# Kernel optimization log

Hardware: AMD Instinct MI355X
Metric: run time of the kernel (lower is better)

The kernel has to match this reference:

```python
import jax, jax.numpy as jnp
import numpy as np

B, N, F, H = 8, 2048, 64, 1

def setup_inputs() -> dict:
    key = jax.random.key(0)
    k1, k2, k3, k4 = jax.random.split(key, 4)
    return {
        "encode": jax.random.normal(k1, (B, N, F), dtype=jnp.float32),
        "kernel": jax.random.normal(k2, (F, H, F), dtype=jnp.float32) * 0.1,
        "attn_kernel_self": jax.random.normal(k3, (F, H, 1), dtype=jnp.float32) * 0.1,
        "attn_kernel_neighs": jax.random.normal(k4, (F, H, 1), dtype=jnp.float32) * 0.1,
    }

def reference(encode, kernel, attn_kernel_self, attn_kernel_neighs):
    # project: [B,N,F] x [F,H,F] -> [B,N,H,F]
    h = jnp.einsum('bni,iho->bnho', encode, kernel)
    # per-node scalar scores: [B,N,H,1]
    a_self = jnp.einsum('bnhi,iho->bnho', h, attn_kernel_self)
    a_neigh = jnp.einsum('bnhi,iho->bnho', h, attn_kernel_neighs)
    # transpose last three axes (...ABC -> ...CBA): [B,1,H,N]
    a_neigh_t = jnp.transpose(a_neigh, (0, 3, 2, 1))
    # broadcast-sum -> [B,N,H,N] dense logits, leaky_relu(alpha=0.2), softmax over neighbors
    logits = jax.nn.leaky_relu(a_self + a_neigh_t, negative_slope=0.2)
    coef = jax.nn.softmax(logits, axis=-1)
    # mean over heads (axis=2) -> [B,N,N]
    return jnp.mean(coef, axis=2)
```

## Files before the change

kernel.cpp:

```cpp
#include <hip/hip_runtime.h>

#define BB 8
#define NN 2048
#define FF 64

typedef float f32x4 __attribute__((ext_vector_type(4)));

__global__ __launch_bounds__(256) void scores_fused(const float* __restrict__ enc,
                                                    const float* __restrict__ kmat,
                                                    const float* __restrict__ aks,
                                                    const float* __restrict__ akn,
                                                    float* __restrict__ S,
                                                    float* __restrict__ T) {
    __shared__ float ws[FF], wn[FF];
    const int tid = threadIdx.x;
    if (tid < FF) {
        float s = 0.f, t = 0.f;
        #pragma unroll
        for (int o = 0; o < FF; ++o) {
            float k = kmat[tid * FF + o];
            s += k * aks[o];
            t += k * akn[o];
        }
        ws[tid] = s;
        wn[tid] = t;
    }
    __syncthreads();

    const int g = blockIdx.x * 256 + tid;
    const f32x4* e4 = (const f32x4*)(enc + (size_t)g * FF);
    const f32x4* w4 = (const f32x4*)ws;
    const f32x4* v4 = (const f32x4*)wn;
    float s = 0.f, t = 0.f;
    #pragma unroll
    for (int j = 0; j < FF / 4; ++j) {
        f32x4 e = e4[j];
        f32x4 w = w4[j];
        f32x4 v = v4[j];
        s += e.x * w.x + e.y * w.y + e.z * w.z + e.w * w.w;
        t += e.x * v.x + e.y * v.y + e.z * v.z + e.w * v.w;
    }
    S[g] = s;
    T[g] = t;
}

__device__ __forceinline__ float waveMax(float v) {
    #pragma unroll
    for (int o = 32; o > 0; o >>= 1) v = fmaxf(v, __shfl_xor(v, o, 64));
    return v;
}
__device__ __forceinline__ float waveSum(float v) {
    #pragma unroll
    for (int o = 32; o > 0; o >>= 1) v += __shfl_xor(v, o, 64);
    return v;
}

__global__ __launch_bounds__(256) void softmax_kernel(const float* __restrict__ S,
                                                      const float* __restrict__ T,
                                                      float* __restrict__ out) {
    const int wave = threadIdx.x >> 6;
    const int lane = threadIdx.x & 63;
    const int row  = blockIdx.x * 4 + wave;
    const int b    = row >> 11;

    const float s = S[row];
    const f32x4* t4 = (const f32x4*)(T + (size_t)b * NN);

    auto lk = [](float x) { return x > 0.f ? x : 0.2f * x; };

    f32x4 l[8];
    float m = -3.4e38f;
    #pragma unroll
    for (int j = 0; j < 8; ++j) {
        f32x4 t = t4[lane + 64 * j];
        l[j].x = lk(s + t.x); l[j].y = lk(s + t.y);
        l[j].z = lk(s + t.z); l[j].w = lk(s + t.w);
        m = fmaxf(m, fmaxf(fmaxf(l[j].x, l[j].y), fmaxf(l[j].z, l[j].w)));
    }
    m = waveMax(m);

    float ls = 0.f;
    #pragma unroll
    for (int j = 0; j < 8; ++j) {
        l[j].x = __expf(l[j].x - m); l[j].y = __expf(l[j].y - m);
        l[j].z = __expf(l[j].z - m); l[j].w = __expf(l[j].w - m);
        ls += (l[j].x + l[j].y) + (l[j].z + l[j].w);
    }
    ls = waveSum(ls);
    const float inv = 1.f / ls;

    f32x4* o4 = (f32x4*)(out + (size_t)row * NN);
    #pragma unroll
    for (int j = 0; j < 8; ++j) {
        f32x4 o;
        o.x = l[j].x * inv; o.y = l[j].y * inv;
        o.z = l[j].z * inv; o.w = l[j].w * inv;
        __builtin_nontemporal_store(o, &o4[lane + 64 * j]);
    }
}

extern "C" void kernel_launch(void* const* d_in, const int* in_sizes, int n_in,
                              void* d_out, int out_size, void* d_ws, size_t ws_size,
                              hipStream_t stream) {
    const float* enc  = (const float*)d_in[0];
    const float* kmat = (const float*)d_in[1];
    const float* aks  = (const float*)d_in[2];
    const float* akn  = (const float*)d_in[3];
    float* out = (float*)d_out;

    float* W = (float*)d_ws;
    float* S = W;
    float* T = W + BB * NN;

    scores_fused<<<BB * NN / 256, 256, 0, stream>>>(enc, kmat, aks, akn, S, T);
    softmax_kernel<<<BB * NN / 4, 256, 0, stream>>>(S, T, out);
}
```

Baseline: 33.32 us.

## Reuse T row across four rows per wave and derive max analytically

Each wave now handles four output rows, loading the per-batch T vector once and reusing it. Because leaky_relu is monotonic, the row max is computed analytically as lk(s + max(T)), which removes the per-row max reduction. The scores are prescaled by log2(e) so exp2 can be used directly. The kernel is dominated by the 128MB of output writes, so the gain from less compute may be limited, and the grid shrinks by a factor of four.

```diff
diff --git a/kernel.cpp b/kernel.cpp
--- a/kernel.cpp
+++ b/kernel.cpp
@@ -3,6 +3,7 @@
 #define BB 8
 #define NN 2048
 #define FF 64
+#define LOG2E 1.4426950408889634f
 
 typedef float f32x4 __attribute__((ext_vector_type(4)));
 
@@ -40,8 +41,8 @@
         s += e.x * w.x + e.y * w.y + e.z * w.z + e.w * w.w;
         t += e.x * v.x + e.y * v.y + e.z * v.z + e.w * v.w;
     }
-    S[g] = s;
-    T[g] = t;
+    S[g] = s * LOG2E;
+    T[g] = t * LOG2E;
 }
 
 __device__ __forceinline__ float waveMax(float v) {
@@ -54,48 +55,56 @@
     for (int o = 32; o > 0; o >>= 1) v += __shfl_xor(v, o, 64);
     return v;
 }
+__device__ __forceinline__ float lk(float x) { return fmaxf(x, 0.2f * x); }
+
+#define ROWS_PER_WAVE 4
 
 __global__ __launch_bounds__(256) void softmax_kernel(const float* __restrict__ S,
                                                       const float* __restrict__ T,
                                                       float* __restrict__ out) {
     const int wave = threadIdx.x >> 6;
     const int lane = threadIdx.x & 63;
-    const int row  = blockIdx.x * 4 + wave;
-    const int b    = row >> 11;
+    const int row0 = (blockIdx.x * 4 + wave) * ROWS_PER_WAVE;
+    const int b    = row0 >> 11;
 
-    const float s = S[row];
     const f32x4* t4 = (const f32x4*)(T + (size_t)b * NN);
 
-    auto lk = [](float x) { return x > 0.f ? x : 0.2f * x; };
-
-    f32x4 l[8];
-    float m = -3.4e38f;
+    f32x4 t[8];
+    float tm = -3.4e38f;
     #pragma unroll
     for (int j = 0; j < 8; ++j) {
-        f32x4 t = t4[lane + 64 * j];
-        l[j].x = lk(s + t.x); l[j].y = lk(s + t.y);
-        l[j].z = lk(s + t.z); l[j].w = lk(s + t.w);
-        m = fmaxf(m, fmaxf(fmaxf(l[j].x, l[j].y), fmaxf(l[j].z, l[j].w)));
+        t[j] = t4[lane + 64 * j];
+        tm = fmaxf(tm, fmaxf(fmaxf(t[j].x, t[j].y), fmaxf(t[j].z, t[j].w)));
     }
-    m = waveMax(m);
+    const float tmax = waveMax(tm);
 
-    float ls = 0.f;
     #pragma unroll
-    for (int j = 0; j < 8; ++j) {
-        l[j].x = __expf(l[j].x - m); l[j].y = __expf(l[j].y - m);
-        l[j].z = __expf(l[j].z - m); l[j].w = __expf(l[j].w - m);
-        ls += (l[j].x + l[j].y) + (l[j].z + l[j].w);
-    }
-    ls = waveSum(ls);
-    const float inv = 1.f / ls;
+    for (int r = 0; r < ROWS_PER_WAVE; ++r) {
+        const int row = row0 + r;
+        const float s = S[row];
+        const float M = lk(s + tmax);
 
-    f32x4* o4 = (f32x4*)(out + (size_t)row * NN);
-    #pragma unroll
-    for (int j = 0; j < 8; ++j) {
-        f32x4 o;
-        o.x = l[j].x * inv; o.y = l[j].y * inv;
-        o.z = l[j].z * inv; o.w = l[j].w * inv;
-        __builtin_nontemporal_store(o, &o4[lane + 64 * j]);
+        f32x4 e[8];
+        float ls = 0.f;
+        #pragma unroll
+        for (int j = 0; j < 8; ++j) {
+            e[j].x = __builtin_exp2f(lk(s + t[j].x) - M);
+            e[j].y = __builtin_exp2f(lk(s + t[j].y) - M);
+            e[j].z = __builtin_exp2f(lk(s + t[j].z) - M);
+            e[j].w = __builtin_exp2f(lk(s + t[j].w) - M);
+            ls += (e[j].x + e[j].y) + (e[j].z + e[j].w);
+        }
+        ls = waveSum(ls);
+        const float inv = 1.f / ls;
+
+        f32x4* o4 = (f32x4*)(out + (size_t)row * NN);
+        #pragma unroll
+        for (int j = 0; j < 8; ++j) {
+            f32x4 o;
+            o.x = e[j].x * inv; o.y = e[j].y * inv;
+            o.z = e[j].z * inv; o.w = e[j].w * inv;
+            __builtin_nontemporal_store(o, &o4[lane + 64 * j]);
+        }
     }
 }
 
@@ -113,5 +122,5 @@
     float* T = W + BB * NN;
 
     scores_fused<<<BB * NN / 256, 256, 0, stream>>>(enc, kmat, aks, akn, S, T);
-    softmax_kernel<<<BB * NN / 4, 256, 0, stream>>>(S, T, out);
+    softmax_kernel<<<BB * NN / (4 * ROWS_PER_WAVE), 256, 0, stream>>>(S, T, out);
 }
```

New measurement: 34.16 us. 2.5% more time.
